# Optimization experiments

Hardware: AMD Instinct MI355X
Metric: run time of the kernel (lower is better)

## Reference

```python
import jax, jax.numpy as jnp
import numpy as np

B, NM, NB, Z, H, K = 1024, 20000, 25000, 64, 256, 20
BETA = 0.1
LOG2PI = float(np.log(2.0 * np.pi))


def _log_normal(x, m, v):
    D = x.shape[-1]
    return (-0.5 * D * LOG2PI
            - 0.5 * jnp.sum(jnp.log(v), axis=-1)
            - 0.5 * jnp.sum((x - m) ** 2 / v, axis=-1))


def _kl_gmm(z, q_m, q_logv, p_m, p_logv):
    log_q = _log_normal(z, q_m, jnp.exp(q_logv))                               # [B]
    lp = _log_normal(z[:, None, :], p_m[None], jnp.exp(p_logv)[None])          # [B,K]
    log_p = jax.scipy.special.logsumexp(lp, axis=1) - jnp.log(float(p_m.shape[0]))
    return jnp.sum(log_q - log_p)


def _dist2(x, y):
    # ||x_i - y_j||_2^2, expanded form (avoids the [R,C,D] broadcast of the torch code)
    x2 = jnp.sum(x * x, axis=1, keepdims=True)
    y2 = jnp.sum(y * y, axis=1, keepdims=True)
    return x2 + y2.T - 2.0 * (x @ y.T)


def _distance_gmm(mu_s, mu_d, lv_s, lv_d):
    return _dist2(mu_s, mu_d) + _dist2(jnp.exp(0.5 * lv_s), jnp.exp(0.5 * lv_d)) + 1e-6


def _cost_mat(cost_s, cost_t, tran):
    f1 = jnp.sum(cost_s ** 2, axis=1, keepdims=True) / cost_s.shape[0]  # [ns,1]
    f2 = jnp.sum(cost_t ** 2, axis=1, keepdims=True) / cost_t.shape[0]  # [nt,1]
    return f1 + f2.T - 2.0 * (cost_s @ tran @ cost_t.T)


def _fgw(mu, z_mu, logvar, z_logvar):
    c_post = _distance_gmm(mu, mu, logvar, logvar)
    c_prior = _distance_gmm(z_mu, z_mu, z_logvar, z_logvar)
    c_pp = _distance_gmm(mu, z_mu, logvar, z_logvar)
    ns, nt = c_post.shape[0], c_prior.shape[0]
    p_s = jnp.ones((ns, 1), c_post.dtype) / ns
    p_t = jnp.ones((nt, 1), c_post.dtype) / nt

    def compute_tran(c_post, c_prior, c_pp):
        def outer(carry, _):
            tran, dual = carry
            cost = BETA * _cost_mat(c_post, c_prior, tran) + (1.0 - BETA) * c_pp
            kernel = jnp.exp(-cost / jnp.max(jnp.abs(cost))) * tran
            b = p_t / (kernel.T @ dual)

            def inner(c2, _):
                dual, b = c2
                dual = p_s / (kernel @ b)
                b = p_t / (kernel.T @ dual)
                return (dual, b), None

            (dual, b), _ = jax.lax.scan(inner, (dual, b), None, length=5)
            tran = (dual @ b.T) * kernel
            return (tran, dual), None

        init = (jnp.ones((ns, nt), c_post.dtype) / (ns * nt),
                jnp.ones((ns, 1), c_post.dtype) / ns)
        (tran, _), _ = jax.lax.scan(outer, init, None, length=10)
        return jnp.where(jnp.any(jnp.isnan(tran)),
                         jnp.ones((ns, nt), tran.dtype) / (ns * nt), tran)

    # torch detaches tran before the final cost, so cut all gradient through the loop
    tran = jax.lax.stop_gradient(compute_tran(c_post, c_prior, c_pp))
    cost = BETA * _cost_mat(c_post, c_prior, tran) + (1.0 - BETA) * c_pp
    return jnp.sum(cost * tran)


def _forward(batch_user_x, batch_user_y, p_mu_a, p_logv_a, p_mu_b, p_logv_b,
             eps_x, eps_y, eps_xr, eps_yr,
             W1a, b1a, W21a, b21a, W22a, b22a, W3a, b3a, W4a, b4a,
             W1b, b1b, W21b, b21b, W22b, b22b, W3b, b3b, W4b, b4b):
    def enc_a(x):
        h = jax.nn.relu(x @ W1a + b1a)
        return h @ W21a + b21a, h @ W22a + b22a

    def dec_a(z):
        return jax.nn.relu(z @ W3a + b3a) @ W4a + b4a

    def enc_b(x):
        h = jax.nn.relu(x @ W1b + b1b)
        return h @ W21b + b21b, h @ W22b + b22b

    def dec_b(z):
        return jax.nn.relu(z @ W3b + b3b) @ W4b + b4b

    # dropout rate = 0.0 -> identity
    mu_a, logvar_a = enc_a(batch_user_x)
    z_x = mu_a + eps_x * jnp.exp(0.5 * logvar_a)
    preds_x = dec_a(z_x)
    mu_b, logvar_b = enc_b(batch_user_y)
    z_y = mu_b + eps_y * jnp.exp(0.5 * logvar_b)
    preds_y = dec_b(z_y)

    gmm_reg_loss_a = _kl_gmm(z_x, mu_a, logvar_a, p_mu_a, p_logv_a)
    gmm_reg_loss_b = _kl_gmm(z_y, mu_b, logvar_b, p_mu_b, p_logv_b)
    align_global_loss = _fgw(mu_b, mu_a, logvar_b, logvar_a)

    preds_x2y = dec_b(z_x)
    preds_y2x = dec_a(z_y)
    m_xr, lv_xr = enc_b(preds_x2y)
    feature_x_r = m_xr + eps_xr * jnp.exp(0.5 * lv_xr)
    m_yr, lv_yr = enc_a(preds_y2x)
    feature_y_r = m_yr + eps_yr * jnp.exp(0.5 * lv_yr)

    cyc_loss_x = jnp.linalg.norm(z_x - feature_x_r)
    cyc_loss_y = jnp.linalg.norm(z_y - feature_y_r)
    return (preds_x, preds_y, preds_x2y, preds_y2x, z_x, z_y,
            gmm_reg_loss_a, gmm_reg_loss_b, feature_x_r, feature_y_r,
            align_global_loss, cyc_loss_x, cyc_loss_y)


def setup_inputs() -> dict:
    key = jax.random.key(0)
    ks = jax.random.split(key, 24)

    def nrm(i, shape, s=1.0):
        return jax.random.normal(ks[i], shape, dtype=jnp.float32) * s

    return {
        "user_1": jax.random.randint(ks[0], (B,), 0, 100000),
        "user_2": jax.random.randint(ks[1], (B,), 0, 100000),
        "batch_user_x": jax.random.uniform(ks[2], (B, NM), dtype=jnp.float32),
        "batch_user_y": jax.random.uniform(ks[3], (B, NB), dtype=jnp.float32),
        "p_mu_a": nrm(4, (K, Z)), "p_logv_a": nrm(5, (K, Z), 0.1),
        "p_mu_b": nrm(6, (K, Z)), "p_logv_b": nrm(7, (K, Z), 0.1),
        "eps_x": nrm(8, (B, Z)), "eps_y": nrm(9, (B, Z)),
        "eps_xr": nrm(10, (B, Z)), "eps_yr": nrm(11, (B, Z)),
        "W1a": nrm(12, (NM, H), 0.02), "b1a": jnp.zeros((H,), jnp.float32),
        "W21a": nrm(13, (H, Z), 0.02), "b21a": jnp.zeros((Z,), jnp.float32),
        "W22a": nrm(14, (H, Z), 0.02), "b22a": jnp.zeros((Z,), jnp.float32),
        "W3a": nrm(15, (Z, H), 0.02), "b3a": jnp.zeros((H,), jnp.float32),
        "W4a": nrm(16, (H, NM), 0.02), "b4a": jnp.zeros((NM,), jnp.float32),
        "W1b": nrm(17, (NB, H), 0.02), "b1b": jnp.zeros((H,), jnp.float32),
        "W21b": nrm(18, (H, Z), 0.02), "b21b": jnp.zeros((Z,), jnp.float32),
        "W22b": nrm(19, (H, Z), 0.02), "b22b": jnp.zeros((Z,), jnp.float32),
        "W3b": nrm(20, (Z, H), 0.02), "b3b": jnp.zeros((H,), jnp.float32),
        "W4b": nrm(21, (H, NB), 0.02), "b4b": jnp.zeros((NB,), jnp.float32),
    }


def reference(user_1, user_2, batch_user_x, batch_user_y, p_mu_a, p_logv_a, p_mu_b, p_logv_b,
              eps_x, eps_y, eps_xr, eps_yr,
              W1a, b1a, W21a, b21a, W22a, b22a, W3a, b3a, W4a, b4a,
              W1b, b1b, W21b, b21b, W22b, b22b, W3b, b3b, W4b, b4b):
    # user_1/user_2 are unused by the torch forward as well
    return _forward(batch_user_x, batch_user_y, p_mu_a, p_logv_a, p_mu_b, p_logv_b,
                    eps_x, eps_y, eps_xr, eps_yr,
                    W1a, b1a, W21a, b21a, W22a, b22a, W3a, b3a, W4a, b4a,
                    W1b, b1b, W21b, b21b, W22b, b22b, W3b, b3b, W4b, b4b)
```

## Files before the change

kernel.cpp:

```cpp
#include <hip/hip_runtime.h>


#define DEVI __device__ __forceinline__

typedef __attribute__((ext_vector_type(4))) float  f32x4;
typedef __attribute__((ext_vector_type(4))) short  s16x4;
typedef __attribute__((ext_vector_type(8))) short  s16x8;
typedef __attribute__((ext_vector_type(8))) __bf16 bf16x8;

DEVI short f2bf(float f) {
  unsigned u = __float_as_uint(f);
  u += 0x7fffu + ((u >> 16) & 1u);
  return (short)(u >> 16);
}
DEVI float bf2f(unsigned short u) { return __uint_as_float(((unsigned)u) << 16); }

DEVI f32x4 mfma16(bf16x8 a, bf16x8 b, f32x4 c) {
  return __builtin_amdgcn_mfma_f32_16x16x32_bf16(a, b, c, 0, 0, 0);
}

struct GemmArgs {
  const float* Af;
  const unsigned short* Bt;
  float* outF;
  const float* bias;
  float* partials;
  int M, N, K;
  int lda, ldbt, ldc;
  int totSteps, nSplits;
};

enum { EPI_PARTIAL, EPI_BIAS, EPI_BF16, EPI_COST, EPI_LOSS };

template<int BM, int BN, int WR, int WC, int EPI>
DEVI void gemm_body(const GemmArgs g)
{
  constexpr int BK = 64, BKP = 72;
  constexpr int NT = WR * WC * 64;
  __shared__ short As[BM * BKP];
  __shared__ short Bs[BN * BKP];

  const int m0 = blockIdx.x * BM;
  int n0 = 0, kb0 = 0, kb1 = g.K, split = 0;
  if constexpr (EPI == EPI_PARTIAL) {
    split = blockIdx.y;
    int s0 = (split * g.totSteps) / g.nSplits;
    int s1 = ((split + 1) * g.totSteps) / g.nSplits;
// ... 72 lines not shown
        } else {
          if (gn < g.N) g.outF[(size_t)gm * g.ldc + gn] = v + g.bias[gn];
        }
      }
    }
  }
}

template<int BM, int BN, int WR, int WC, int EPI>
__global__ __launch_bounds__(WR*WC*64)
void k_gemm2(GemmArgs g0, GemmArgs g1)
{
  gemm_body<BM, BN, WR, WC, EPI>(blockIdx.z ? g1 : g0);
}

struct FgwGemmArgs {
  const unsigned short* A;
  const unsigned short* Bt;
  unsigned short* U;
  float* cost;
  const float* f1;
  const float* f2;
  const float* cpp;
  const float* tran;
  unsigned* mx;
  float* loss;
  float* braw;
};

template<int EPI>
__global__ __launch_bounds__(256)
void k_fgw_gemm(FgwGemmArgs a)
{
  __shared__ short As[64 * 72];
  __shared__ short Bs[64 * 72];
  __shared__ float red[4];

  const int bid = blockIdx.x, tid = threadIdx.x;
  const int lane = tid & 63, wv = tid >> 6;
  const int wr = wv & 1, wc = wv >> 1;
  const int m0 = (bid >> 4) * 64, n0 = (bid & 15) * 64;

  if constexpr (EPI == EPI_COST) {
    if (bid == 0) {
      #pragma unroll
      for (int i = 0; i < 4; ++i) a.braw[tid + 256 * i] = 0.f;
    }
  }

  f32x4 acc[2][2];
  #pragma unroll
  for (int i = 0; i < 2; ++i)
    #pragma unroll
    for (int j = 0; j < 2; ++j) acc[i][j] = f32x4{0.f, 0.f, 0.f, 0.f};

  for (int kb = 0; kb < 1024; kb += 64) {
    #pragma unroll
    for (int i = 0; i < 2; ++i) {
      int idx = tid + 256 * i;
      int r = idx >> 3, q = idx & 7;
      *(s16x8*)&As[r * 72 + 8 * q] = *(const s16x8*)&a.A [(size_t)(m0 + r) * 1024 + kb + 8 * q];
      *(s16x8*)&Bs[r * 72 + 8 * q] = *(const s16x8*)&a.Bt[(size_t)(n0 + r) * 1024 + kb + 8 * q];
    }
    __syncthreads();
    #pragma unroll
    for (int s = 0; s < 2; ++s) {
      const int ko = 32 * s + 8 * (lane >> 4);
      bf16x8 a0 = *(const bf16x8*)&As[(wr * 32 +      (lane & 15)) * 72 + ko];
      bf16x8 a1 = *(const bf16x8*)&As[(wr * 32 + 16 + (lane & 15)) * 72 + ko];
      bf16x8 b0 = *(const bf16x8*)&Bs[(wc * 32 +      (lane & 15)) * 72 + ko];
      bf16x8 b1 = *(const bf16x8*)&Bs[(wc * 32 + 16 + (lane & 15)) * 72 + ko];
      acc[0][0] = mfma16(a0, b0, acc[0][0]);
      acc[1][0] = mfma16(a1, b0, acc[1][0]);
      acc[0][1] = mfma16(a0, b1, acc[0][1]);
      acc[1][1] = mfma16(a1, b1, acc[1][1]);
    }
    __syncthreads();
  }

  float lred = 0.f;
  #pragma unroll
  for (int fm = 0; fm < 2; ++fm) {
    #pragma unroll
    for (int fn = 0; fn < 2; ++fn) {
      #pragma unroll
      for (int p = 0; p < 4; ++p) {
        int gm = m0 + wr * 32 + fm * 16 + (lane >> 4) * 4 + p;
        int gn = n0 + wc * 32 + fn * 16 + (lane & 15);
        float v = acc[fm][fn][p];
        size_t o = (size_t)gm * 1024 + gn;
        if constexpr (EPI == EPI_BF16) {
          a.U[o] = (unsigned short)f2bf(v);
        } else {
          float c = 0.1f * (a.f1[gm] + a.f2[gn] - 2.f * v) + 0.9f * a.cpp[o];
          if constexpr (EPI == EPI_COST) {
            a.cost[o] = c;
            lred = fmaxf(lred, fabsf(c));
          } else {
            lred += c * a.tran[o];
          }
        }
      }
    }
  }
  if constexpr (EPI != EPI_BF16) {
    #pragma unroll
    for (int off = 32; off; off >>= 1) {
      float t = __shfl_xor(lred, off, 64);
      lred = (EPI == EPI_COST) ? fmaxf(lred, t) : (lred + t);
    }
    if (lane == 0) red[wv] = lred;
    __syncthreads();
    if (tid == 0) {
      if constexpr (EPI == EPI_COST) {
        float t = fmaxf(fmaxf(red[0], red[1]), fmaxf(red[2], red[3]));
        atomicMax(a.mx, __float_as_uint(t));
      } else {
        atomicAdd(a.loss, red[0] + red[1] + red[2] + red[3]);
      }
    }
  }
}

struct FP {
  const float* mu[2]; const float* lv[2];
  unsigned short* F[2]; float* n[2];
};
__global__ __launch_bounds__(64)
void k_featprep(FP a)
{
  const int y = blockIdx.y;
  const int i = blockIdx.x;
  const int t = threadIdx.x;
  float v0 = a.mu[y][(size_t)i * 64 + t];
  float v1 = expf(0.5f * a.lv[y][(size_t)i * 64 + t]);
  unsigned short u0 = (unsigned short)f2bf(v0);
  unsigned short u1 = (unsigned short)f2bf(v1);
  unsigned short* Fr = a.F[y] + (size_t)i * 128;
  Fr[t] = u0;
  Fr[64 + t] = u1;
  float r0 = bf2f(u0), r1 = bf2f(u1);
  float p = r0 * r0 + r1 * r1;
  #pragma unroll
  for (int o = 32; o; o >>= 1) p += __shfl_xor(p, o, 64);
  if (t == 0) a.n[y][i] = p;
}

struct DistMMArgs {
  const unsigned short* Fx[3]; const unsigned short* Fy[3];
  const float* nx[3]; const float* ny[3];
  unsigned short* outB[2]; float* outF; float* frow[2];
};
__global__ __launch_bounds__(256)
void k_distmm(DistMMArgs a)
{
  __shared__ short As[64 * 72];
  __shared__ short Bs[64 * 72];
  const int z = blockIdx.y;
  const int bid = blockIdx.x, tid = threadIdx.x;
  const int lane = tid & 63, wv = tid >> 6;
// ... 70 lines not shown
        v += __shfl_xor(v, 8, 64);
        rp[fm][p] = v;
      }
    if ((lane & 15) == 0) {
      #pragma unroll
      for (int fm = 0; fm < 2; ++fm)
        #pragma unroll
        for (int p = 0; p < 4; ++p) {
          int gm = m0 + wr * 32 + fm * 16 + (lane >> 4) * 4 + p;
          atomicAdd(&a.frow[z][gm], rp[fm][p] * (1.f / 1024.f));
        }
    }
  }
}

__global__ __launch_bounds__(256)
void k_kbuild(const float* cost, const float* tran, const unsigned* mxbits,
              const float* draw, float* braw, float* K, float* KT)
{
  __shared__ float t[64 * 65];
  __shared__ float dualS[64];
  __shared__ float csum[4][64];
  const int r0 = blockIdx.x * 64, c0 = blockIdx.y * 64;
  const int tid = threadIdx.x;
  const float inv = 1.f / __uint_as_float(*mxbits);
  const float PS = 1.f / 1024.f;
  if (tid < 64) dualS[tid] = PS / draw[r0 + tid];
  __syncthreads();
  float colpart = 0.f;
  #pragma unroll
  for (int i = 0; i < 16; ++i) {
    int idx = tid + 256 * i;
    int r = idx >> 6, c = idx & 63;
    size_t o = (size_t)(r0 + r) * 1024 + (c0 + c);
    float v = expf(-cost[o] * inv) * tran[o];
    K[o] = v;
    t[r * 65 + c] = v;
    colpart += v * dualS[r];
  }
  csum[tid >> 6][tid & 63] = colpart;
  __syncthreads();
  #pragma unroll
  for (int i = 0; i < 16; ++i) {
    int idx = tid + 256 * i;
    int c = idx >> 6, r = idx & 63;
    KT[(size_t)(c0 + c) * 1024 + (r0 + r)] = t[r * 65 + c];
  }
  if (tid < 64)
    atomicAdd(&braw[c0 + tid],
              csum[0][tid] + csum[1][tid] + csum[2][tid] + csum[3][tid]);
}

__global__ __launch_bounds__(256)
void k_matvec(const float* M, const float* xraw, float* yraw)
{
  const int r = blockIdx.x * 4 + (threadIdx.x >> 6);
  const int lane = threadIdx.x & 63;
  const float C = 1.f / 1024.f;
  const f32x4* row = (const f32x4*)(M + (size_t)r * 1024);
  const f32x4* xv  = (const f32x4*)xraw;
  float s = 0.f;
  #pragma unroll
  for (int q = 0; q < 4; ++q) {
    f32x4 a = row[lane + 64 * q];
    f32x4 x = xv [lane + 64 * q];
    s += a.x * (C / x.x) + a.y * (C / x.y) + a.z * (C / x.z) + a.w * (C / x.w);
  }
  #pragma unroll
  for (int o = 32; o; o >>= 1) s += __shfl_xor(s, o, 64);
  if (lane == 0) yraw[r] = s;
}

__global__ __launch_bounds__(256)
void k_tranupd(const float* K, const float* draw, const float* braw,
               float* tran, unsigned short* tranT, unsigned* flag, int check)
{
  __shared__ float t[64 * 65];
  __shared__ float dualS[64], bS[64];
  const int r0 = blockIdx.x * 64, c0 = blockIdx.y * 64;
  const int tid = threadIdx.x;
  const float P = 1.f / 1024.f;
  if (tid < 64) dualS[tid] = P / draw[r0 + tid];
  else if (tid < 128) bS[tid - 64] = P / braw[c0 + tid - 64];
  __syncthreads();
  unsigned bad = 0;
  #pragma unroll
  for (int i = 0; i < 16; ++i) {
    int idx = tid + 256 * i;
    int r = idx >> 6, c = idx & 63;
    size_t o = (size_t)(r0 + r) * 1024 + (c0 + c);
    float v = dualS[r] * bS[c] * K[o];
    tran[o] = v;
    t[r * 65 + c] = v;
    if (v != v) bad = 1u;
  }
  __syncthreads();
  #pragma unroll
  for (int i = 0; i < 16; ++i) {
    int idx = tid + 256 * i;
    int c = idx >> 6, r = idx & 63;
    tranT[(size_t)(c0 + c) * 1024 + (r0 + r)] = (unsigned short)f2bf(t[r * 65 + c]);
  }
  if (check && bad) atomicOr(flag, 1u);
}

struct T4 { const float* in[4]; unsigned short* out[4]; int R[4], C[4], nx[4], nt[4]; };
__global__ void k_transpose4(T4 d)
{
  __shared__ float t[64][65];
  const int z = blockIdx.y;
  const int tile = blockIdx.x;
  if (tile >= d.nt[z]) return;
  const int R = d.R[z], C = d.C[z];
  const int r0 = (tile % d.nx[z]) * 64, c0 = (tile / d.nx[z]) * 64;
  const float* in = d.in[z];
  unsigned short* out = d.out[z];
  const int tid = threadIdx.x;
  #pragma unroll
  for (int i = 0; i < 16; ++i) {
    int idx = tid + 256 * i;
// ... 54 lines not shown
  float s = 0.f;
  for (int k = lane * 8; k < K; k += 512) {
    s16x8 w = *(const s16x8*)&wrow[k];
    f32x4 v0 = *(const f32x4*)&b4[k];
    f32x4 v1 = *(const f32x4*)&b4[k + 4];
    s += v0.x * bf2f((unsigned short)w[0]) + v0.y * bf2f((unsigned short)w[1])
       + v0.z * bf2f((unsigned short)w[2]) + v0.w * bf2f((unsigned short)w[3])
       + v1.x * bf2f((unsigned short)w[4]) + v1.y * bf2f((unsigned short)w[5])
       + v1.z * bf2f((unsigned short)w[6]) + v1.w * bf2f((unsigned short)w[7]);
  }
  #pragma unroll
  for (int o = 32; o; o >>= 1) s += __shfl_xor(s, o, 64);
  if (lane == 0) a.bc[y][c] = s + a.b1[y][c];
}

struct Red2 { const float* partials[2]; const float* bias[2]; float* h[2]; int ns; };
__global__ void k_reduce2(Red2 a)
{
  const int y = blockIdx.y;
  int idx = blockIdx.x * 256 + threadIdx.x;
  float s = a.bias[y][idx & 255];
  const float* P = a.partials[y];
  for (int p = 0; p < a.ns; ++p) s += P[(size_t)p * (1024 * 256) + idx];
  a.h[y][idx] = fmaxf(s, 0.f);
}

struct EH2 {
  const float* h[2]; const float* W21[2]; const float* b21[2];
  const float* W22[2]; const float* b22[2]; const float* eps[2];
  float* mu[2]; float* lv[2]; float* zO[2];
};
__global__ void k_enc_head2(EH2 a)
{
  __shared__ float hrow[256];
  __shared__ float res[128];
  const int y = blockIdx.y;
  const int i = blockIdx.x;
  const int t = threadIdx.x;
  hrow[t]       = a.h[y][(size_t)i * 256 + t];
  hrow[t + 128] = a.h[y][(size_t)i * 256 + t + 128];
  __syncthreads();
  const int c = t & 63;
  const float* W = (t < 64) ? a.W21[y] : a.W22[y];
  float acc = (t < 64) ? a.b21[y][c] : a.b22[y][c];
  #pragma unroll 8
  for (int j = 0; j < 256; ++j) acc += hrow[j] * W[j * 64 + c];
  res[t] = acc;
  __syncthreads();
  if (t < 64) {
    float mu = res[t], lv = res[64 + t];
    a.mu[y][(size_t)i * 64 + t] = mu;
    a.lv[y][(size_t)i * 64 + t] = lv;
    a.zO[y][(size_t)i * 64 + t] = mu + a.eps[y][(size_t)i * 64 + t] * expf(0.5f * lv);
  }
}

struct RencArgs {
  const float* hd[2]; const unsigned short* WcT[2]; const float* bc[2];
  const float* W21[2]; const float* b21[2]; const float* W22[2]; const float* b22[2];
  const float* eps[2]; float* fout[2];
};
__global__ void k_renc_head(RencArgs a)
{
  __shared__ float hdrow[256];
  __shared__ float hr[256];
  __shared__ float res[128];
  const int y = blockIdx.y;
  const int i = blockIdx.x;
// ... 34 lines not shown
__global__ void k_dec_head4(DH4 a)
{
  __shared__ float zrow[64];
  const int y = blockIdx.y;
  const int i = blockIdx.x;
  const int t = threadIdx.x;
  if (t < 64) zrow[t] = a.z[y][(size_t)i * 64 + t];
  __syncthreads();
  const float* W3 = a.W3[y];
  float acc = a.b3[y][t];
  #pragma unroll
  for (int d = 0; d < 64; ++d) acc += zrow[d] * W3[d * 256 + t];
  a.hd[y][(size_t)i * 256 + t] = fmaxf(acc, 0.f);
}

__global__ void k_init(float* tran, unsigned short* tranT, float* draw, float* braw,
                       float* f1, float* f2, unsigned* mx, unsigned* nanflag,
                       float* cyc, float* ga, float* gb, float* al)
{
  const int bid = blockIdx.x, tid = threadIdx.x;
  const float v = 1.f / (1024.f * 1024.f);
  const unsigned short vb = (unsigned short)f2bf(v);
  const size_t base = (size_t)bid * 1024;
  #pragma unroll
  for (int i = 0; i < 4; ++i) {
    tran [base + tid + 256 * i] = v;
    tranT[base + tid + 256 * i] = vb;
  }
  if (bid == 0) {
    #pragma unroll
    for (int i = 0; i < 4; ++i) {
      int k = tid + 256 * i;
      draw[k] = 1.f; braw[k] = 0.f; f1[k] = 0.f; f2[k] = 0.f;
    }
    if (tid < 16) mx[tid] = 0u;
    if (tid == 0) { *nanflag = 0u; cyc[0] = 0.f; cyc[1] = 0.f; *ga = 0.f; *gb = 0.f; *al = 0.f; }
  }
}

__global__ void k_nanfix(float* tran, unsigned short* tranT, const unsigned* flag)
{
  if (*flag == 0u) return;
  const int bid = blockIdx.x, tid = threadIdx.x;
  const float v = 1.f / (1024.f * 1024.f);
  const unsigned short vb = (unsigned short)f2bf(v);
  const size_t base = (size_t)bid * 1024;
  #pragma unroll
  for (int i = 0; i < 4; ++i) {
    tran [base + tid + 256 * i] = v;
    tranT[base + tid + 256 * i] = vb;
  }
}

struct G2 {
  const float* z[2]; const float* mu[2]; const float* lv[2];
  const float* pmu[2]; const float* plv[2]; float* o[2];
};
__global__ void k_gmm2(G2 a)
{
  const int y = blockIdx.y;
  const int i = blockIdx.x;
  const int d = threadIdx.x;
  const float zd = a.z[y][(size_t)i * 64 + d];
  const float m  = a.mu[y][(size_t)i * 64 + d];
  const float l  = a.lv[y][(size_t)i * 64 + d];
  float t = l + (zd - m) * (zd - m) * expf(-l);
// ... 78 lines not shown
  char* w = (char*)d_ws;
  size_t off = 0;
  auto alloc = [&](size_t bytes) -> void* {
    void* p = w + off;
    off += (bytes + 255) & ~(size_t)255;
    return p;
  };
  unsigned short* Wt1a = (unsigned short*)alloc((size_t)256 * 20000 * 2);
  unsigned short* Wt1b = (unsigned short*)alloc((size_t)256 * 25000 * 2);
  unsigned short* W4ta = (unsigned short*)alloc((size_t)20000 * 256 * 2);
  unsigned short* W4tb = (unsigned short*)alloc((size_t)25000 * 256 * 2);
  unsigned short* WcTa = (unsigned short*)alloc((size_t)256 * 256 * 2);
  unsigned short* WcTb = (unsigned short*)alloc((size_t)256 * 256 * 2);
  float* bca  = (float*)alloc(256 * 4);
  float* bcb  = (float*)alloc(256 * 4);
  float* h0   = (float*)alloc((size_t)1024 * 256 * 4);
  float* h1   = (float*)alloc((size_t)1024 * 256 * 4);
  float* mu_a = (float*)alloc(1024 * 64 * 4);
  float* lv_a = (float*)alloc(1024 * 64 * 4);
  float* mu_b = (float*)alloc(1024 * 64 * 4);
  float* lv_b = (float*)alloc(1024 * 64 * 4);
  float* f1   = (float*)alloc(1024 * 4);
  float* f2   = (float*)alloc(1024 * 4);
  unsigned* mx      = (unsigned*)alloc(16 * 4);
  unsigned* nanflag = (unsigned*)alloc(256);
  float* cyc  = (float*)alloc(256);
  float* draw = (float*)alloc(1024 * 4);
  float* braw = (float*)alloc(1024 * 4);
  unsigned short* Fb = (unsigned short*)alloc((size_t)1024 * 128 * 2);
  unsigned short* Fa = (unsigned short*)alloc((size_t)1024 * 128 * 2);
  float* nb = (float*)alloc(1024 * 4);
  float* na = (float*)alloc(1024 * 4);
  char* arena = (char*)alloc((size_t)32 * 1024 * 1024);
  float* partials = (float*)arena;
  size_t ao = 0;
  auto aalloc = [&](size_t bytes) -> void* {
    void* p = arena + ao;
    ao += (bytes + 255) & ~(size_t)255;
    return p;
  };
  unsigned short* cpostB  = (unsigned short*)aalloc((size_t)1024 * 1024 * 2);
  unsigned short* cpriorB = (unsigned short*)aalloc((size_t)1024 * 1024 * 2);
  float* cpp  = (float*)aalloc((size_t)1024 * 1024 * 4);
  float* tran = (float*)aalloc((size_t)1024 * 1024 * 4);
  unsigned short* tranT = (unsigned short*)aalloc((size_t)1024 * 1024 * 2);
  unsigned short* Umat  = (unsigned short*)aalloc((size_t)1024 * 1024 * 2);
  float* cost  = (float*)aalloc((size_t)1024 * 1024 * 4);
  float* Kmat  = (float*)aalloc((size_t)1024 * 1024 * 4);
  float* KTmat = (float*)aalloc((size_t)1024 * 1024 * 4);
  float* hd0 = (float*)(arena);
  float* hd1 = (float*)(arena + (size_t)1024 * 256 * 4);
  float* hd2 = (float*)(arena + (size_t)2 * 1024 * 256 * 4);
  float* hd3 = (float*)(arena + (size_t)3 * 1024 * 256 * 4);

  {
    T4 d{};
    d.in[0] = W1a; d.out[0] = Wt1a; d.R[0] = 20000; d.C[0] = 256;
    d.in[1] = W1b; d.out[1] = Wt1b; d.R[1] = 25000; d.C[1] = 256;
    d.in[2] = W4a; d.out[2] = W4ta; d.R[2] = 256;   d.C[2] = 20000;
    d.in[3] = W4b; d.out[3] = W4tb; d.R[3] = 256;   d.C[3] = 25000;
    for (int z = 0; z < 4; ++z) {
      d.nx[z] = (d.R[z] + 63) / 64;
      d.nt[z] = d.nx[z] * ((d.C[z] + 63) / 64);
    }
    k_transpose4<<<dim3(1564, 4), 256, 0, stream>>>(d);
  }

  k_init<<<1024, 256, 0, stream>>>(tran, tranT, draw, braw, f1, f2, mx, nanflag,
                                   cyc, out + GMM_A, out + GMM_B, out + ALIGN);

  {
    GemmArgs ga{}, gb{};
    ga.Af = W4a; ga.Bt = Wt1a; ga.partials = partials;
    ga.M = 256; ga.N = 256; ga.K = 20000; ga.lda = 20000; ga.ldbt = 20000;
    ga.totSteps = 313; ga.nSplits = 32;
    gb = ga;
    gb.Af = W4b; gb.Bt = Wt1b; gb.partials = partials + (size_t)32 * 65536;
    gb.K = 25000; gb.lda = 25000; gb.ldbt = 25000; gb.totSteps = 391;
    k_gemm2<128, 256, 4, 4, EPI_PARTIAL><<<dim3(2, 32, 2), 1024, 0, stream>>>(ga, gb);
    k_wcomb_reduce<<<dim3(4, 4, 2), 256, 0, stream>>>(partials, WcTa, WcTb);
    BcArgs bc{};
    bc.b4[0] = b4a; bc.Wt1[0] = Wt1a; bc.b1[0] = b1a; bc.bc[0] = bca; bc.K[0] = 20000;
    bc.b4[1] = b4b; bc.Wt1[1] = Wt1b; bc.b1[1] = b1b; bc.bc[1] = bcb; bc.K[1] = 25000;
    k_bcvec<<<dim3(64, 2), 256, 0, stream>>>(bc);
  }

  {
    GemmArgs ga{}, gb{};
    ga.Af = X; ga.Bt = Wt1a; ga.partials = partials;
    ga.M = 1024; ga.N = 256; ga.K = 20000; ga.lda = 20000; ga.ldbt = 20000;
    ga.totSteps = 313; ga.nSplits = 16;
    gb = ga;
    gb.Af = Y; gb.Bt = Wt1b; gb.partials = partials + (size_t)16 * 1024 * 256;
    gb.K = 25000; gb.lda = 25000; gb.ldbt = 25000; gb.totSteps = 391;
    k_gemm2<128, 256, 4, 4, EPI_PARTIAL><<<dim3(8, 16, 2), 1024, 0, stream>>>(ga, gb);
    Red2 r{};
    r.partials[0] = partials; r.partials[1] = partials + (size_t)16 * 1024 * 256;
    r.bias[0] = b1a; r.bias[1] = b1b; r.h[0] = h0; r.h[1] = h1; r.ns = 16;
    k_reduce2<<<dim3(1024, 2), 256, 0, stream>>>(r);
    EH2 e{};
    e.h[0] = h0; e.W21[0] = W21a; e.b21[0] = b21a; e.W22[0] = W22a; e.b22[0] = b22a;
    e.eps[0] = epsx; e.mu[0] = mu_a; e.lv[0] = lv_a; e.zO[0] = out + Z_X;
    e.h[1] = h1; e.W21[1] = W21b; e.b21[1] = b21b; e.W22[1] = W22b; e.b22[1] = b22b;
    e.eps[1] = epsy; e.mu[1] = mu_b; e.lv[1] = lv_b; e.zO[1] = out + Z_Y;
    k_enc_head2<<<dim3(1024, 2), 128, 0, stream>>>(e);
  }

  {
    G2 g{};
    g.z[0] = out + Z_X; g.mu[0] = mu_a; g.lv[0] = lv_a; g.pmu[0] = pmua; g.plv[0] = plva;
    g.o[0] = out + GMM_A;
    g.z[1] = out + Z_Y; g.mu[1] = mu_b; g.lv[1] = lv_b; g.pmu[1] = pmub; g.plv[1] = plvb;
    g.o[1] = out + GMM_B;
    k_gmm2<<<dim3(1024, 2), 64, 0, stream>>>(g);
  }

  {
    FP fp{};
    fp.mu[0] = mu_b; fp.lv[0] = lv_b; fp.F[0] = Fb; fp.n[0] = nb;
    fp.mu[1] = mu_a; fp.lv[1] = lv_a; fp.F[1] = Fa; fp.n[1] = na;
    k_featprep<<<dim3(1024, 2), 64, 0, stream>>>(fp);
    DistMMArgs dm{};
    dm.Fx[0] = Fb; dm.Fy[0] = Fb; dm.nx[0] = nb; dm.ny[0] = nb;
    dm.Fx[1] = Fa; dm.Fy[1] = Fa; dm.nx[1] = na; dm.ny[1] = na;
    dm.Fx[2] = Fb; dm.Fy[2] = Fa; dm.nx[2] = nb; dm.ny[2] = na;
    dm.outB[0] = cpostB; dm.outB[1] = cpriorB; dm.outF = cpp;
    dm.frow[0] = f1; dm.frow[1] = f2;
    k_distmm<<<dim3(256, 3), 256, 0, stream>>>(dm);
  }
  FgwGemmArgs fg{};
  fg.f1 = f1; fg.f2 = f2; fg.cpp = cpp; fg.loss = out + ALIGN; fg.braw = braw;
  for (int it = 0; it < 10; ++it) {
    fg.A = cpostB; fg.Bt = tranT; fg.U = Umat;
    k_fgw_gemm<EPI_BF16><<<256, 256, 0, stream>>>(fg);
    fg.A = Umat; fg.Bt = cpriorB; fg.cost = cost; fg.mx = mx + it;
    k_fgw_gemm<EPI_COST><<<256, 256, 0, stream>>>(fg);
    k_kbuild<<<dim3(16, 16), 256, 0, stream>>>(cost, tran, mx + it, draw, braw, Kmat, KTmat);
    for (int r = 0; r < 5; ++r) {
      k_matvec<<<256, 256, 0, stream>>>(Kmat,  braw, draw);
      k_matvec<<<256, 256, 0, stream>>>(KTmat, draw, braw);
    }
    k_tranupd<<<dim3(16, 16), 256, 0, stream>>>(Kmat, draw, braw, tran, tranT,
                                                nanflag, it == 9 ? 1 : 0);
  }
  k_nanfix<<<1024, 256, 0, stream>>>(tran, tranT, nanflag);
  fg.A = cpostB; fg.Bt = tranT; fg.U = Umat;
  k_fgw_gemm<EPI_BF16><<<256, 256, 0, stream>>>(fg);
  fg.A = Umat; fg.Bt = cpriorB; fg.tran = tran;
  k_fgw_gemm<EPI_LOSS><<<256, 256, 0, stream>>>(fg);

  {
    DH4 d{};
    d.z[0] = out + Z_X; d.W3[0] = W3a; d.b3[0] = b3a; d.hd[0] = hd0;
    d.z[1] = out + Z_Y; d.W3[1] = W3a; d.b3[1] = b3a; d.hd[1] = hd1;
    d.z[2] = out + Z_Y; d.W3[2] = W3b; d.b3[2] = b3b; d.hd[2] = hd2;
    d.z[3] = out + Z_X; d.W3[3] = W3b; d.b3[3] = b3b; d.hd[3] = hd3;
    k_dec_head4<<<dim3(1024, 4), 256, 0, stream>>>(d);
  }

  {
    RencArgs r{};
    r.hd[0] = hd3; r.WcT[0] = WcTb; r.bc[0] = bcb;
    r.W21[0] = W21b; r.b21[0] = b21b; r.W22[0] = W22b; r.b22[0] = b22b;
// ... 31 lines not shown
```

Measured before the change: 1.549 ms.

## Eliminate explicit transport matrix by folding dual scalings into Sinkhorn consumers

Removes the per-iteration tran/tranT materialization kernel and instead represents the transport plan implicitly as diag(dual)·K·diag(b). The scalings are applied on the fly in the first FGW GEMM's tile loads (reading fp32 KT and converting to bf16), in kbuild, and in the loss epilogue. The NaN fallback becomes a final scan kernel. It also fuses the encoder partial reduction, heads and feature prep into one kernel, and shrinks init. This cuts several full 1024x1024 passes and launches per iteration, but the GEMM B-operand now loads fp32 data and converts it in the inner loop.

```diff
diff --git a/kernel.cpp b/kernel.cpp
--- a/kernel.cpp
+++ b/kernel.cpp
@@ -7,6 +7,9 @@
 typedef __attribute__((ext_vector_type(4))) short  s16x4;
 typedef __attribute__((ext_vector_type(8))) short  s16x8;
 typedef __attribute__((ext_vector_type(8))) __bf16 bf16x8;
+
+#define PS (1.f / 1024.f)
+#define UNIF (1.f / (1024.f * 1024.f))
 
 DEVI short f2bf(float f) {
   unsigned u = __float_as_uint(f);
@@ -30,7 +33,7 @@
   int totSteps, nSplits;
 };
 
-enum { EPI_PARTIAL, EPI_BIAS, EPI_BF16, EPI_COST, EPI_LOSS };
+enum { EPI_PARTIAL, EPI_BIAS, EPI_COST, EPI_LOSS };
 
 template<int BM, int BN, int WR, int WC, int EPI>
 DEVI void gemm_body(const GemmArgs g)
@@ -133,53 +136,68 @@
   gemm_body<BM, BN, WR, WC, EPI>(blockIdx.z ? g1 : g0);
 }
 
-struct FgwGemmArgs {
+struct G1Args {
   const unsigned short* A;
-  const unsigned short* Bt;
+  const float* KT;
+  const float* dinv;
+  const float* braw;
   unsigned short* U;
-  float* cost;
-  const float* f1;
-  const float* f2;
-  const float* cpp;
-  const float* tran;
-  unsigned* mx;
-  float* loss;
-  float* braw;
+  const unsigned* nflag;
+  int mode;
 };
 
-template<int EPI>
 __global__ __launch_bounds__(256)
-void k_fgw_gemm(FgwGemmArgs a)
+void k_fgw_g1(G1Args a)
 {
   __shared__ short As[64 * 72];
   __shared__ short Bs[64 * 72];
-  __shared__ float red[4];
+  const bool uni = (a.mode == 0) || (a.mode == 2 && *a.nflag != 0u);
 
   const int bid = blockIdx.x, tid = threadIdx.x;
   const int lane = tid & 63, wv = tid >> 6;
   const int wr = wv & 1, wc = wv >> 1;
   const int m0 = (bid >> 4) * 64, n0 = (bid & 15) * 64;
 
-  if constexpr (EPI == EPI_COST) {
-    if (bid == 0) {
-      #pragma unroll
-      for (int i = 0; i < 4; ++i) a.braw[tid + 256 * i] = 0.f;
-    }
-  }
-
   f32x4 acc[2][2];
   #pragma unroll
   for (int i = 0; i < 2; ++i)
     #pragma unroll
     for (int j = 0; j < 2; ++j) acc[i][j] = f32x4{0.f, 0.f, 0.f, 0.f};
+
+  const short ub = f2bf(UNIF);
 
   for (int kb = 0; kb < 1024; kb += 64) {
     #pragma unroll
     for (int i = 0; i < 2; ++i) {
       int idx = tid + 256 * i;
       int r = idx >> 3, q = idx & 7;
-      *(s16x8*)&As[r * 72 + 8 * q] = *(const s16x8*)&a.A [(size_t)(m0 + r) * 1024 + kb + 8 * q];
-      *(s16x8*)&Bs[r * 72 + 8 * q] = *(const s16x8*)&a.Bt[(size_t)(n0 + r) * 1024 + kb + 8 * q];
+      s16x8 av = *(const s16x8*)&a.A[(size_t)(m0 + r) * 1024 + kb + 8 * q];
+      if (!uni) {
+        f32x4 d0 = *(const f32x4*)&a.dinv[kb + 8 * q];
+        f32x4 d1 = *(const f32x4*)&a.dinv[kb + 8 * q + 4];
+        s16x8 o;
+        o[0] = f2bf(bf2f((unsigned short)av[0]) * d0.x);
+        o[1] = f2bf(bf2f((unsigned short)av[1]) * d0.y);
+        o[2] = f2bf(bf2f((unsigned short)av[2]) * d0.z);
+        o[3] = f2bf(bf2f((unsigned short)av[3]) * d0.w);
+        o[4] = f2bf(bf2f((unsigned short)av[4]) * d1.x);
+        o[5] = f2bf(bf2f((unsigned short)av[5]) * d1.y);
+        o[6] = f2bf(bf2f((unsigned short)av[6]) * d1.z);
+        o[7] = f2bf(bf2f((unsigned short)av[7]) * d1.w);
+        av = o;
+      }
+      *(s16x8*)&As[r * 72 + 8 * q] = av;
+      s16x8 bv;
+      if (uni) {
+        #pragma unroll
+        for (int j = 0; j < 8; ++j) bv[j] = ub;
+      } else {
+        f32x4 k0 = *(const f32x4*)&a.KT[(size_t)(n0 + r) * 1024 + kb + 8 * q];
+        f32x4 k1 = *(const f32x4*)&a.KT[(size_t)(n0 + r) * 1024 + kb + 8 * q + 4];
+        bv[0] = f2bf(k0.x); bv[1] = f2bf(k0.y); bv[2] = f2bf(k0.z); bv[3] = f2bf(k0.w);
+        bv[4] = f2bf(k1.x); bv[5] = f2bf(k1.y); bv[6] = f2bf(k1.z); bv[7] = f2bf(k1.w);
+      }
+      *(s16x8*)&Bs[r * 72 + 8 * q] = bv;
     }
     __syncthreads();
     #pragma unroll
@@ -197,72 +215,208 @@
     __syncthreads();
   }
 
-  float lred = 0.f;
   #pragma unroll
   for (int fm = 0; fm < 2; ++fm) {
     #pragma unroll
     for (int fn = 0; fn < 2; ++fn) {
+      int gn = n0 + wc * 32 + fn * 16 + (lane & 15);
+      float bs = uni ? 1.f : (PS / a.braw[gn]);
       #pragma unroll
       for (int p = 0; p < 4; ++p) {
         int gm = m0 + wr * 32 + fm * 16 + (lane >> 4) * 4 + p;
-        int gn = n0 + wc * 32 + fn * 16 + (lane & 15);
+        float v = acc[fm][fn][p];
+        a.U[(size_t)gm * 1024 + gn] = (unsigned short)f2bf(uni ? v : bs * v);
+      }
+    }
+  }
+}
+
+struct FgwGemmArgs {
+  const unsigned short* A;
+  const unsigned short* Bt;
+  float* cost;
+  const float* f1;
+  const float* f2;
+  const float* cpp;
+  unsigned* mx;
+  float* loss;
+  float* braw2;
+  const float* Kf;
+  const float* dinv;
+  const float* brawv;
+  const unsigned* nflag;
+};
+
+template<int EPI>
+__global__ __launch_bounds__(256)
+void k_fgw_gemm(FgwGemmArgs a)
+{
+  __shared__ short As[64 * 72];
+  __shared__ short Bs[64 * 72];
+  __shared__ float red[4];
+
+  const int bid = blockIdx.x, tid = threadIdx.x;
+  const int lane = tid & 63, wv = tid >> 6;
+  const int wr = wv & 1, wc = wv >> 1;
+  const int m0 = (bid >> 4) * 64, n0 = (bid & 15) * 64;
+
+  if constexpr (EPI == EPI_COST) {
+    if (bid == 0) {
+      #pragma unroll
+      for (int i = 0; i < 4; ++i) a.braw2[tid + 256 * i] = 0.f;
+    }
+  }
+
+  f32x4 acc[2][2];
+  #pragma unroll
+  for (int i = 0; i < 2; ++i)
+    #pragma unroll
+    for (int j = 0; j < 2; ++j) acc[i][j] = f32x4{0.f, 0.f, 0.f, 0.f};
+
+  for (int kb = 0; kb < 1024; kb += 64) {
+    #pragma unroll
+    for (int i = 0; i < 2; ++i) {
+      int idx = tid + 256 * i;
+      int r = idx >> 3, q = idx & 7;
+      *(s16x8*)&As[r * 72 + 8 * q] = *(const s16x8*)&a.A [(size_t)(m0 + r) * 1024 + kb + 8 * q];
+      *(s16x8*)&Bs[r * 72 + 8 * q] = *(const s16x8*)&a.Bt[(size_t)(n0 + r) * 1024 + kb + 8 * q];
+    }
+    __syncthreads();
+    #pragma unroll
+    for (int s = 0; s < 2; ++s) {
+      const int ko = 32 * s + 8 * (lane >> 4);
+      bf16x8 a0 = *(const bf16x8*)&As[(wr * 32 +      (lane & 15)) * 72 + ko];
+      bf16x8 a1 = *(const bf16x8*)&As[(wr * 32 + 16 + (lane & 15)) * 72 + ko];
+      bf16x8 b0 = *(const bf16x8*)&Bs[(wc * 32 +      (lane & 15)) * 72 + ko];
+      bf16x8 b1 = *(const bf16x8*)&Bs[(wc * 32 + 16 + (lane & 15)) * 72 + ko];
+      acc[0][0] = mfma16(a0, b0, acc[0][0]);
+      acc[1][0] = mfma16(a1, b0, acc[1][0]);
+      acc[0][1] = mfma16(a0, b1, acc[0][1]);
+      acc[1][1] = mfma16(a1, b1, acc[1][1]);
+    }
+    __syncthreads();
+  }
+
+  bool uni = false;
+  if constexpr (EPI == EPI_LOSS) uni = (*a.nflag != 0u);
+
+  float lred = 0.f;
+  #pragma unroll
+  for (int fm = 0; fm < 2; ++fm) {
+    #pragma unroll
+    for (int fn = 0; fn < 2; ++fn) {
+      int gn = n0 + wc * 32 + fn * 16 + (lane & 15);
+      float bs = 0.f;
+      if constexpr (EPI == EPI_LOSS) bs = uni ? 0.f : (PS / a.brawv[gn]);
+      #pragma unroll
+      for (int p = 0; p < 4; ++p) {
+        int gm = m0 + wr * 32 + fm * 16 + (lane >> 4) * 4 + p;
         float v = acc[fm][fn][p];
         size_t o = (size_t)gm * 1024 + gn;
-        if constexpr (EPI == EPI_BF16) {
-          a.U[o] = (unsigned short)f2bf(v);
+        float c = 0.1f * (a.f1[gm] + a.f2[gn] - 2.f * v) + 0.9f * a.cpp[o];
+        if constexpr (EPI == EPI_COST) {
+          a.cost[o] = c;
+          lred = fmaxf(lred, fabsf(c));
         } else {
-          float c = 0.1f * (a.f1[gm] + a.f2[gn] - 2.f * v) + 0.9f * a.cpp[o];
-          if constexpr (EPI == EPI_COST) {
-            a.cost[o] = c;
-            lred = fmaxf(lred, fabsf(c));
-          } else {
-            lred += c * a.tran[o];
-          }
+          float trec = uni ? UNIF : (a.dinv[gm] * bs) * a.Kf[o];
+          lred += c * trec;
         }
       }
     }
   }
-  if constexpr (EPI != EPI_BF16) {
-    #pragma unroll
-    for (int off = 32; off; off >>= 1) {
-      float t = __shfl_xor(lred, off, 64);
-      lred = (EPI == EPI_COST) ? fmaxf(lred, t) : (lred + t);
-    }
-    if (lane == 0) red[wv] = lred;
-    __syncthreads();
-    if (tid == 0) {
-      if constexpr (EPI == EPI_COST) {
-        float t = fmaxf(fmaxf(red[0], red[1]), fmaxf(red[2], red[3]));
-        atomicMax(a.mx, __float_as_uint(t));
-      } else {
-        atomicAdd(a.loss, red[0] + red[1] + red[2] + red[3]);
-      }
-    }
-  }
-}
-
-struct FP {
-  const float* mu[2]; const float* lv[2];
-  unsigned short* F[2]; float* n[2];
-};
-__global__ __launch_bounds__(64)
-void k_featprep(FP a)
-{
-  const int y = blockIdx.y;
-  const int i = blockIdx.x;
-  const int t = threadIdx.x;
-  float v0 = a.mu[y][(size_t)i * 64 + t];
-  float v1 = expf(0.5f * a.lv[y][(size_t)i * 64 + t]);
-  unsigned short u0 = (unsigned short)f2bf(v0);
-  unsigned short u1 = (unsigned short)f2bf(v1);
-  unsigned short* Fr = a.F[y] + (size_t)i * 128;
-  Fr[t] = u0;
-  Fr[64 + t] = u1;
-  float r0 = bf2f(u0), r1 = bf2f(u1);
-  float p = r0 * r0 + r1 * r1;
-  #pragma unroll
-  for (int o = 32; o; o >>= 1) p += __shfl_xor(p, o, 64);
-  if (t == 0) a.n[y][i] = p;
+  #pragma unroll
+  for (int off = 32; off; off >>= 1) {
+    float t = __shfl_xor(lred, off, 64);
+    lred = (EPI == EPI_COST) ? fmaxf(lred, t) : (lred + t);
+  }
+  if (lane == 0) red[wv] = lred;
+  __syncthreads();
+  if (tid == 0) {
+    if constexpr (EPI == EPI_COST) {
+      float t = fmaxf(fmaxf(red[0], red[1]), fmaxf(red[2], red[3]));
+      atomicMax(a.mx, __float_as_uint(t));
+    } else {
+      atomicAdd(a.loss, red[0] + red[1] + red[2] + red[3]);
+    }
+  }
+}
+
+__global__ __launch_bounds__(256)
+void k_kbuild(const float* cost, const unsigned* mxbits, float* K, float* KT,
+              const float* dinv, const float* brawOld, float* braw2, int uniform)
+{
+  __shared__ float tt[64 * 65];
+  __shared__ float dS[64];
+  __shared__ float bS[64];
+  __shared__ float csum[4][64];
+  const int r0 = blockIdx.x * 64, c0 = blockIdx.y * 64;
+  const int tid = threadIdx.x;
+  const float inv = 1.f / __uint_as_float(*mxbits);
+  if (tid < 64) dS[tid] = dinv[r0 + tid];
+  else if (tid >= 64 && tid < 128 && !uniform) bS[tid - 64] = PS / brawOld[c0 + tid - 64];
+  __syncthreads();
+  float colp = 0.f;
+  #pragma unroll
+  for (int i = 0; i < 16; ++i) {
+    int idx = tid + 256 * i;
+    int r = idx >> 6, c = idx & 63;
+    size_t o = (size_t)(r0 + r) * 1024 + (c0 + c);
+    float trec = uniform ? UNIF : (dS[r] * bS[c]) * K[o];
+    float v = expf(-cost[o] * inv) * trec;
+    K[o] = v;
+    tt[r * 65 + c] = v;
+    colp += v * dS[r];
+  }
+  csum[tid >> 6][tid & 63] = colp;
+  __syncthreads();
+  #pragma unroll
+  for (int i = 0; i < 16; ++i) {
+    int idx = tid + 256 * i;
+    int c = idx >> 6, r = idx & 63;
+    KT[(size_t)(c0 + c) * 1024 + (r0 + r)] = tt[r * 65 + c];
+  }
+  if (tid < 64)
+    atomicAdd(&braw2[c0 + tid],
+              csum[0][tid] + csum[1][tid] + csum[2][tid] + csum[3][tid]);
+}
+
+__global__ __launch_bounds__(256)
+void k_matvec(const float* M, const float* xraw, float* yraw, float* invOut)
+{
+  const int r = blockIdx.x * 4 + (threadIdx.x >> 6);
+  const int lane = threadIdx.x & 63;
+  const int wv = threadIdx.x >> 6;
+  const f32x4* row = (const f32x4*)(M + (size_t)r * 1024);
+  const f32x4* xv  = (const f32x4*)xraw;
+  float s = 0.f;
+  #pragma unroll
+  for (int q = 0; q < 4; ++q) {
+    f32x4 a = row[lane + 64 * q];
+    f32x4 x = xv [lane + 64 * q];
+    f32x4 iv;
+    iv.x = PS / x.x; iv.y = PS / x.y; iv.z = PS / x.z; iv.w = PS / x.w;
+    if (invOut && blockIdx.x == 0 && wv == 0)
+      *(f32x4*)&invOut[4 * (lane + 64 * q)] = iv;
+    s += a.x * iv.x + a.y * iv.y + a.z * iv.z + a.w * iv.w;
+  }
+  #pragma unroll
+  for (int o = 32; o; o >>= 1) s += __shfl_xor(s, o, 64);
+  if (lane == 0) yraw[r] = s;
+}
+
+__global__ __launch_bounds__(256)
+void k_nanscan(const float* K, const float* dinv, const float* braw, unsigned* flag)
+{
+  unsigned bad = 0;
+  const int base = blockIdx.x * 256 + threadIdx.x;
+  #pragma unroll
+  for (int i = 0; i < 16; ++i) {
+    int idx = base + 65536 * i;
+    int r = idx >> 10, c = idx & 1023;
+    float v = (dinv[r] * (PS / braw[c])) * K[idx];
+    if (v != v) bad = 1u;
+  }
+  if (bad) atomicOr(flag, 1u);
 }
 
 struct DistMMArgs {
@@ -363,96 +517,6 @@
   }
 }
 
-__global__ __launch_bounds__(256)
-void k_kbuild(const float* cost, const float* tran, const unsigned* mxbits,
-              const float* draw, float* braw, float* K, float* KT)
-{
-  __shared__ float t[64 * 65];
-  __shared__ float dualS[64];
-  __shared__ float csum[4][64];
-  const int r0 = blockIdx.x * 64, c0 = blockIdx.y * 64;
-  const int tid = threadIdx.x;
-  const float inv = 1.f / __uint_as_float(*mxbits);
-  const float PS = 1.f / 1024.f;
-  if (tid < 64) dualS[tid] = PS / draw[r0 + tid];
-  __syncthreads();
-  float colpart = 0.f;
-  #pragma unroll
-  for (int i = 0; i < 16; ++i) {
-    int idx = tid + 256 * i;
-    int r = idx >> 6, c = idx & 63;
-    size_t o = (size_t)(r0 + r) * 1024 + (c0 + c);
-    float v = expf(-cost[o] * inv) * tran[o];
-    K[o] = v;
-    t[r * 65 + c] = v;
-    colpart += v * dualS[r];
-  }
-  csum[tid >> 6][tid & 63] = colpart;
-  __syncthreads();
-  #pragma unroll
-  for (int i = 0; i < 16; ++i) {
-    int idx = tid + 256 * i;
-    int c = idx >> 6, r = idx & 63;
-    KT[(size_t)(c0 + c) * 1024 + (r0 + r)] = t[r * 65 + c];
-  }
-  if (tid < 64)
-    atomicAdd(&braw[c0 + tid],
-              csum[0][tid] + csum[1][tid] + csum[2][tid] + csum[3][tid]);
-}
-
-__global__ __launch_bounds__(256)
-void k_matvec(const float* M, const float* xraw, float* yraw)
-{
-  const int r = blockIdx.x * 4 + (threadIdx.x >> 6);
-  const int lane = threadIdx.x & 63;
-  const float C = 1.f / 1024.f;
-  const f32x4* row = (const f32x4*)(M + (size_t)r * 1024);
-  const f32x4* xv  = (const f32x4*)xraw;
-  float s = 0.f;
-  #pragma unroll
-  for (int q = 0; q < 4; ++q) {
-    f32x4 a = row[lane + 64 * q];
-    f32x4 x = xv [lane + 64 * q];
-    s += a.x * (C / x.x) + a.y * (C / x.y) + a.z * (C / x.z) + a.w * (C / x.w);
-  }
-  #pragma unroll
-  for (int o = 32; o; o >>= 1) s += __shfl_xor(s, o, 64);
-  if (lane == 0) yraw[r] = s;
-}
-
-__global__ __launch_bounds__(256)
-void k_tranupd(const float* K, const float* draw, const float* braw,
-               float* tran, unsigned short* tranT, unsigned* flag, int check)
-{
-  __shared__ float t[64 * 65];
-  __shared__ float dualS[64], bS[64];
-  const int r0 = blockIdx.x * 64, c0 = blockIdx.y * 64;
-  const int tid = threadIdx.x;
-  const float P = 1.f / 1024.f;
-  if (tid < 64) dualS[tid] = P / draw[r0 + tid];
-  else if (tid < 128) bS[tid - 64] = P / braw[c0 + tid - 64];
-  __syncthreads();
-  unsigned bad = 0;
-  #pragma unroll
-  for (int i = 0; i < 16; ++i) {
-    int idx = tid + 256 * i;
-    int r = idx >> 6, c = idx & 63;
-    size_t o = (size_t)(r0 + r) * 1024 + (c0 + c);
-    float v = dualS[r] * bS[c] * K[o];
-    tran[o] = v;
-    t[r * 65 + c] = v;
-    if (v != v) bad = 1u;
-  }
-  __syncthreads();
-  #pragma unroll
-  for (int i = 0; i < 16; ++i) {
-    int idx = tid + 256 * i;
-    int c = idx >> 6, r = idx & 63;
-    tranT[(size_t)(c0 + c) * 1024 + (r0 + r)] = (unsigned short)f2bf(t[r * 65 + c]);
-  }
-  if (check && bad) atomicOr(flag, 1u);
-}
-
 struct T4 { const float* in[4]; unsigned short* out[4]; int R[4], C[4], nx[4], nt[4]; };
 __global__ void k_transpose4(T4 d)
 {
@@ -537,44 +601,54 @@
   if (lane == 0) a.bc[y][c] = s + a.b1[y][c];
 }
 
-struct Red2 { const float* partials[2]; const float* bias[2]; float* h[2]; int ns; };
-__global__ void k_reduce2(Red2 a)
-{
-  const int y = blockIdx.y;
-  int idx = blockIdx.x * 256 + threadIdx.x;
-  float s = a.bias[y][idx & 255];
-  const float* P = a.partials[y];
-  for (int p = 0; p < a.ns; ++p) s += P[(size_t)p * (1024 * 256) + idx];
-  a.h[y][idx] = fmaxf(s, 0.f);
-}
-
-struct EH2 {
-  const float* h[2]; const float* W21[2]; const float* b21[2];
+struct EF {
+  const float* partials[2]; const float* bias[2];
+  const float* W21[2]; const float* b21[2];
   const float* W22[2]; const float* b22[2]; const float* eps[2];
   float* mu[2]; float* lv[2]; float* zO[2];
+  unsigned short* F[2]; float* n[2];
 };
-__global__ void k_enc_head2(EH2 a)
+__global__ __launch_bounds__(256)
+void k_enc_fused(EF a)
 {
   __shared__ float hrow[256];
   __shared__ float res[128];
   const int y = blockIdx.y;
   const int i = blockIdx.x;
   const int t = threadIdx.x;
-  hrow[t]       = a.h[y][(size_t)i * 256 + t];
-  hrow[t + 128] = a.h[y][(size_t)i * 256 + t + 128];
-  __syncthreads();
-  const int c = t & 63;
-  const float* W = (t < 64) ? a.W21[y] : a.W22[y];
-  float acc = (t < 64) ? a.b21[y][c] : a.b22[y][c];
-  #pragma unroll 8
-  for (int j = 0; j < 256; ++j) acc += hrow[j] * W[j * 64 + c];
-  res[t] = acc;
+  {
+    float s = a.bias[y][t];
+    const float* P = a.partials[y] + (size_t)i * 256 + t;
+    #pragma unroll
+    for (int p = 0; p < 16; ++p) s += P[(size_t)p * 262144];
+    hrow[t] = fmaxf(s, 0.f);
+  }
+  __syncthreads();
+  if (t < 128) {
+    const int c = t & 63;
+    const float* W = (t < 64) ? a.W21[y] : a.W22[y];
+    float acc = (t < 64) ? a.b21[y][c] : a.b22[y][c];
+    #pragma unroll 8
+    for (int j = 0; j < 256; ++j) acc += hrow[j] * W[j * 64 + c];
+    res[t] = acc;
+  }
   __syncthreads();
   if (t < 64) {
     float mu = res[t], lv = res[64 + t];
     a.mu[y][(size_t)i * 64 + t] = mu;
     a.lv[y][(size_t)i * 64 + t] = lv;
-    a.zO[y][(size_t)i * 64 + t] = mu + a.eps[y][(size_t)i * 64 + t] * expf(0.5f * lv);
+    float sig = expf(0.5f * lv);
+    a.zO[y][(size_t)i * 64 + t] = mu + a.eps[y][(size_t)i * 64 + t] * sig;
+    unsigned short u0 = (unsigned short)f2bf(mu);
+    unsigned short u1 = (unsigned short)f2bf(sig);
+    unsigned short* Fr = a.F[y] + (size_t)i * 128;
+    Fr[t] = u0;
+    Fr[64 + t] = u1;
+    float r0 = bf2f(u0), r1 = bf2f(u1);
+    float p = r0 * r0 + r1 * r1;
+    #pragma unroll
+    for (int o = 32; o; o >>= 1) p += __shfl_xor(p, o, 64);
+    if (t == 0) a.n[y][i] = p;
   }
 }
 
@@ -639,42 +713,14 @@
   a.hd[y][(size_t)i * 256 + t] = fmaxf(acc, 0.f);
 }
 
-__global__ void k_init(float* tran, unsigned short* tranT, float* draw, float* braw,
-                       float* f1, float* f2, unsigned* mx, unsigned* nanflag,
-                       float* cyc, float* ga, float* gb, float* al)
-{
-  const int bid = blockIdx.x, tid = threadIdx.x;
-  const float v = 1.f / (1024.f * 1024.f);
-  const unsigned short vb = (unsigned short)f2bf(v);
-  const size_t base = (size_t)bid * 1024;
-  #pragma unroll
-  for (int i = 0; i < 4; ++i) {
-    tran [base + tid + 256 * i] = v;
-    tranT[base + tid + 256 * i] = vb;
-  }
-  if (bid == 0) {
-    #pragma unroll
-    for (int i = 0; i < 4; ++i) {
-      int k = tid + 256 * i;
-      draw[k] = 1.f; braw[k] = 0.f; f1[k] = 0.f; f2[k] = 0.f;
-    }
-    if (tid < 16) mx[tid] = 0u;
-    if (tid == 0) { *nanflag = 0u; cyc[0] = 0.f; cyc[1] = 0.f; *ga = 0.f; *gb = 0.f; *al = 0.f; }
-  }
-}
-
-__global__ void k_nanfix(float* tran, unsigned short* tranT, const unsigned* flag)
-{
-  if (*flag == 0u) return;
-  const int bid = blockIdx.x, tid = threadIdx.x;
-  const float v = 1.f / (1024.f * 1024.f);
-  const unsigned short vb = (unsigned short)f2bf(v);
-  const size_t base = (size_t)bid * 1024;
-  #pragma unroll
-  for (int i = 0; i < 4; ++i) {
-    tran [base + tid + 256 * i] = v;
-    tranT[base + tid + 256 * i] = vb;
-  }
+__global__ void k_init(float* dinv, float* f1, float* f2, unsigned* mx,
+                       unsigned* nanflag, float* cyc, float* ga, float* gb, float* al)
+{
+  int t = threadIdx.x;
+  dinv[t] = PS;
+  f1[t] = 0.f; f2[t] = 0.f;
+  if (t < 16) mx[t] = 0u;
+  if (t == 0) { *nanflag = 0u; cyc[0] = 0.f; cyc[1] = 0.f; *ga = 0.f; *gb = 0.f; *al = 0.f; }
 }
 
 struct G2 {
@@ -783,8 +829,6 @@
   unsigned short* WcTb = (unsigned short*)alloc((size_t)256 * 256 * 2);
   float* bca  = (float*)alloc(256 * 4);
   float* bcb  = (float*)alloc(256 * 4);
-  float* h0   = (float*)alloc((size_t)1024 * 256 * 4);
-  float* h1   = (float*)alloc((size_t)1024 * 256 * 4);
   float* mu_a = (float*)alloc(1024 * 64 * 4);
   float* lv_a = (float*)alloc(1024 * 64 * 4);
   float* mu_b = (float*)alloc(1024 * 64 * 4);
@@ -796,6 +840,8 @@
   float* cyc  = (float*)alloc(256);
   float* draw = (float*)alloc(1024 * 4);
   float* braw = (float*)alloc(1024 * 4);
+  float* braw2 = (float*)alloc(1024 * 4);
+  float* dinv = (float*)alloc(1024 * 4);
   unsigned short* Fb = (unsigned short*)alloc((size_t)1024 * 128 * 2);
   unsigned short* Fa = (unsigned short*)alloc((size_t)1024 * 128 * 2);
   float* nb = (float*)alloc(1024 * 4);
@@ -811,8 +857,6 @@
   unsigned short* cpostB  = (unsigned short*)aalloc((size_t)1024 * 1024 * 2);
   unsigned short* cpriorB = (unsigned short*)aalloc((size_t)1024 * 1024 * 2);
   float* cpp  = (float*)aalloc((size_t)1024 * 1024 * 4);
-  float* tran = (float*)aalloc((size_t)1024 * 1024 * 4);
-  unsigned short* tranT = (unsigned short*)aalloc((size_t)1024 * 1024 * 2);
   unsigned short* Umat  = (unsigned short*)aalloc((size_t)1024 * 1024 * 2);
   float* cost  = (float*)aalloc((size_t)1024 * 1024 * 4);
   float* Kmat  = (float*)aalloc((size_t)1024 * 1024 * 4);
@@ -835,8 +879,8 @@
     k_transpose4<<<dim3(1564, 4), 256, 0, stream>>>(d);
   }
 
-  k_init<<<1024, 256, 0, stream>>>(tran, tranT, draw, braw, f1, f2, mx, nanflag,
-                                   cyc, out + GMM_A, out + GMM_B, out + ALIGN);
+  k_init<<<1, 1024, 0, stream>>>(dinv, f1, f2, mx, nanflag, cyc,
+                                 out + GMM_A, out + GMM_B, out + ALIGN);
 
   {
     GemmArgs ga{}, gb{};
@@ -863,16 +907,16 @@
     gb.Af = Y; gb.Bt = Wt1b; gb.partials = partials + (size_t)16 * 1024 * 256;
     gb.K = 25000; gb.lda = 25000; gb.ldbt = 25000; gb.totSteps = 391;
     k_gemm2<128, 256, 4, 4, EPI_PARTIAL><<<dim3(8, 16, 2), 1024, 0, stream>>>(ga, gb);
-    Red2 r{};
-    r.partials[0] = partials; r.partials[1] = partials + (size_t)16 * 1024 * 256;
-    r.bias[0] = b1a; r.bias[1] = b1b; r.h[0] = h0; r.h[1] = h1; r.ns = 16;
-    k_reduce2<<<dim3(1024, 2), 256, 0, stream>>>(r);
-    EH2 e{};
-    e.h[0] = h0; e.W21[0] = W21a; e.b21[0] = b21a; e.W22[0] = W22a; e.b22[0] = b22a;
+    EF e{};
+    e.partials[0] = partials; e.partials[1] = partials + (size_t)16 * 1024 * 256;
+    e.bias[0] = b1a; e.bias[1] = b1b;
+    e.W21[0] = W21a; e.b21[0] = b21a; e.W22[0] = W22a; e.b22[0] = b22a;
     e.eps[0] = epsx; e.mu[0] = mu_a; e.lv[0] = lv_a; e.zO[0] = out + Z_X;
-    e.h[1] = h1; e.W21[1] = W21b; e.b21[1] = b21b; e.W22[1] = W22b; e.b22[1] = b22b;
+    e.F[0] = Fa; e.n[0] = na;
+    e.W21[1] = W21b; e.b21[1] = b21b; e.W22[1] = W22b; e.b22[1] = b22b;
     e.eps[1] = epsy; e.mu[1] = mu_b; e.lv[1] = lv_b; e.zO[1] = out + Z_Y;
-    k_enc_head2<<<dim3(1024, 2), 128, 0, stream>>>(e);
+    e.F[1] = Fb; e.n[1] = nb;
+    k_enc_fused<<<dim3(1024, 2), 256, 0, stream>>>(e);
   }
 
   {
@@ -885,10 +929,6 @@
   }
 
   {
-    FP fp{};
-    fp.mu[0] = mu_b; fp.lv[0] = lv_b; fp.F[0] = Fb; fp.n[0] = nb;
-    fp.mu[1] = mu_a; fp.lv[1] = lv_a; fp.F[1] = Fa; fp.n[1] = na;
-    k_featprep<<<dim3(1024, 2), 64, 0, stream>>>(fp);
     DistMMArgs dm{};
     dm.Fx[0] = Fb; dm.Fy[0] = Fb; dm.nx[0] = nb; dm.ny[0] = nb;
     dm.Fx[1] = Fa; dm.Fy[1] = Fa; dm.nx[1] = na; dm.ny[1] = na;
@@ -897,25 +937,29 @@
     dm.frow[0] = f1; dm.frow[1] = f2;
     k_distmm<<<dim3(256, 3), 256, 0, stream>>>(dm);
   }
+  G1Args g1{};
+  g1.A = cpostB; g1.KT = KTmat; g1.dinv = dinv; g1.braw = braw;
+  g1.U = Umat; g1.nflag = nanflag;
   FgwGemmArgs fg{};
-  fg.f1 = f1; fg.f2 = f2; fg.cpp = cpp; fg.loss = out + ALIGN; fg.braw = braw;
+  fg.A = Umat; fg.Bt = cpriorB;
+  fg.f1 = f1; fg.f2 = f2; fg.cpp = cpp; fg.cost = cost;
+  fg.loss = out + ALIGN; fg.braw2 = braw2;
+  fg.Kf = Kmat; fg.dinv = dinv; fg.brawv = braw; fg.nflag = nanflag;
   for (int it = 0; it < 10; ++it) {
-    fg.A = cpostB; fg.Bt = tranT; fg.U = Umat;
-    k_fgw_gemm<EPI_BF16><<<256, 256, 0, stream>>>(fg);
-    fg.A = Umat; fg.Bt = cpriorB; fg.cost = cost; fg.mx = mx + it;
+    g1.mode = (it == 0) ? 0 : 1;
+    k_fgw_g1<<<256, 256, 0, stream>>>(g1);
+    fg.mx = mx + it;
     k_fgw_gemm<EPI_COST><<<256, 256, 0, stream>>>(fg);
-    k_kbuild<<<dim3(16, 16), 256, 0, stream>>>(cost, tran, mx + it, draw, braw, Kmat, KTmat);
+    k_kbuild<<<dim3(16, 16), 256, 0, stream>>>(cost, mx + it, Kmat, KTmat,
+                                               dinv, braw, braw2, it == 0 ? 1 : 0);
     for (int r = 0; r < 5; ++r) {
-      k_matvec<<<256, 256, 0, stream>>>(Kmat,  braw, draw);
-      k_matvec<<<256, 256, 0, stream>>>(KTmat, draw, braw);
-    }
-    k_tranupd<<<dim3(16, 16), 256, 0, stream>>>(Kmat, draw, braw, tran, tranT,
-                                                nanflag, it == 9 ? 1 : 0);
-  }
-  k_nanfix<<<1024, 256, 0, stream>>>(tran, tranT, nanflag);
-  fg.A = cpostB; fg.Bt = tranT; fg.U = Umat;
-  k_fgw_gemm<EPI_BF16><<<256, 256, 0, stream>>>(fg);
-  fg.A = Umat; fg.Bt = cpriorB; fg.tran = tran;
+      k_matvec<<<256, 256, 0, stream>>>(Kmat, r == 0 ? braw2 : braw, draw, nullptr);
+      k_matvec<<<256, 256, 0, stream>>>(KTmat, draw, braw, r == 4 ? dinv : nullptr);
+    }
+  }
+  k_nanscan<<<256, 256, 0, stream>>>(Kmat, dinv, braw, nanflag);
+  g1.mode = 2;
+  k_fgw_g1<<<256, 256, 0, stream>>>(g1);
   k_fgw_gemm<EPI_LOSS><<<256, 256, 0, stream>>>(fg);
 
   {
```

New measurement: 1.582 ms. 2.1% more time.
